# Optimization experiments

Measured on AMD Instinct MI355X. Metric: run time of the kernel, lower is better.

Reference implementation:

```python
import jax, jax.numpy as jnp
import numpy as np

N_NODES = 50000
N_EDGES = 800000
D = 128
BN_EPS = 1e-5


def setup_inputs() -> dict:
    key = jax.random.key(0)
    ks = jax.random.split(key, 8)
    scale = 1.0 / np.sqrt(D)
    return {
        "nfeat": jax.random.normal(ks[0], (N_NODES, D), dtype=jnp.float32),
        "efeat": jax.random.normal(ks[1], (N_EDGES, D), dtype=jnp.float32),
        "src": jax.random.randint(ks[2], (N_EDGES,), 0, N_NODES, dtype=jnp.int32),
        "dst": jax.random.randint(ks[3], (N_EDGES,), 0, N_NODES, dtype=jnp.int32),
        "W1": jax.random.normal(ks[4], (D, D), dtype=jnp.float32) * scale,
        "b1": jnp.zeros((D,), dtype=jnp.float32),
        "gamma": jnp.ones((D,), dtype=jnp.float32),
        "beta": jnp.zeros((D,), dtype=jnp.float32),
        "W2": jax.random.normal(ks[5], (D, D), dtype=jnp.float32) * scale,
        "b2": jnp.zeros((D,), dtype=jnp.float32),
        "We": jax.random.normal(ks[6], (D, D), dtype=jnp.float32) * scale,
        "be": jnp.zeros((D,), dtype=jnp.float32),
    }


def reference(nfeat, efeat, src, dst, W1, b1, gamma, beta, W2, b2, We, be):
    n = nfeat.shape[0]
    # GINConv, sum aggregator, eps=0: h = (1+eps)*x + sum_{j in N(i)} x_j
    agg = jax.ops.segment_sum(nfeat[src], dst, num_segments=n)  # [N, D]
    h = nfeat + agg
    # apply_func: Linear -> BatchNorm1d (training-mode batch stats) -> ReLU -> Linear
    h = h @ W1 + b1
    mu = jnp.mean(h, axis=0)
    var = jnp.mean(jnp.square(h - mu), axis=0)  # biased variance, as BatchNorm uses
    h = gamma * (h - mu) * jax.lax.rsqrt(var + BN_EPS) + beta
    h = jax.nn.relu(h)
    h = h @ W2 + b2
    # edge branch: linear on edge feats, scatter-sum to destination nodes, residual add
    e = efeat @ We + be                                          # [E, D]
    h_e = jax.ops.segment_sum(e, dst, num_segments=n)            # [N, D]
    return h + h_e
```

## Files before the change

### kernel.cpp

```cpp
#include <hip/hip_runtime.h>

#define D 128

typedef __attribute__((ext_vector_type(8))) short bf16x8;
typedef __attribute__((ext_vector_type(4))) float f32x4;

static __device__ __forceinline__ short f2bf(float f) {
    union { float f; unsigned u; } v; v.f = f;
    const unsigned r = v.u + 0x7FFFu + ((v.u >> 16) & 1u);
    return (short)(r >> 16);
}
static __device__ __forceinline__ float bf2f(short s) {
    union { unsigned u; float f; } v;
    v.u = ((unsigned)(unsigned short)s) << 16;
    return v.f;
}

__global__ __launch_bounds__(256) void k_prep(
    const float* __restrict__ nfeat, short* __restrict__ nfb,
    const float* __restrict__ W1, const float* __restrict__ W2,
    const float* __restrict__ We, short* __restrict__ Wt1,
    short* __restrict__ Wt2, short* __restrict__ Wte,
    int* __restrict__ cnt, float* __restrict__ stats,
    int N, int nbConv, int nbW)
{
    const int b = blockIdx.x, t = threadIdx.x;
    if (b < nbConv) {
        const int i = b * 256 + t;
        if (i < (N * D) / 4) {
            const float4 v = ((const float4*)nfeat)[i];
            short4 s;
            s.x = f2bf(v.x); s.y = f2bf(v.y); s.z = f2bf(v.z); s.w = f2bf(v.w);
            ((short4*)nfb)[i] = s;
        }
    } else if (b < nbConv + nbW) {
        const int i = (b - nbConv) * 256 + t;
        const int m = i >> 14;
        const int idx = i & 16383;
        const int k = idx >> 7, n = idx & 127;
        const float* W = (m == 0) ? W1 : (m == 1) ? W2 : We;
        short* Wt = (m == 0) ? Wt1 : (m == 1) ? Wt2 : Wte;
        Wt[n * 128 + k] = f2bf(W[k * 128 + n]);
    } else {
        const int i = (b - nbConv - nbW) * 256 + t;
        if (i * 4 < N) ((int4*)cnt)[i] = make_int4(0, 0, 0, 0);
        if (b == nbConv + nbW && t < 256) stats[t] = 0.f;
    }
}

__global__ void k_hist(const int* __restrict__ dst, int* __restrict__ cnt, int E) {
    const int base = (blockIdx.x * 256 + threadIdx.x) * 4;
    if (base + 3 < E) {
        const int4 d4 = *(const int4*)(dst + base);
        atomicAdd(&cnt[d4.x], 1);
        atomicAdd(&cnt[d4.y], 1);
        atomicAdd(&cnt[d4.z], 1);
        atomicAdd(&cnt[d4.w], 1);
    } else {
        for (int e = base; e < E; ++e) atomicAdd(&cnt[dst[e]], 1);
    }
}

__global__ __launch_bounds__(1024) void k_scan(
    const int* __restrict__ cnt, int* __restrict__ row_ptr,
    int* __restrict__ cursor, float* __restrict__ degf, int N)
{
    __shared__ int ws[17];
    const int t = threadIdx.x, lane = t & 63, wid = t >> 6;
    int carry = 0;
    const int ntiles = (N + 4095) / 4096;
    for (int tile = 0; tile < ntiles; ++tile) {
        const int base = tile * 4096 + t * 4;
        int4 v = make_int4(0, 0, 0, 0);
        if (base + 3 < N) v = *(const int4*)(cnt + base);
        else {
            if (base     < N) v.x = cnt[base];
            if (base + 1 < N) v.y = cnt[base + 1];
            if (base + 2 < N) v.z = cnt[base + 2];
            if (base + 3 < N) v.w = cnt[base + 3];
        }
        const int s = v.x + v.y + v.z + v.w;
        int incl = s;
        #pragma unroll
        for (int off = 1; off < 64; off <<= 1) {
            const int u = __shfl_up(incl, off);
            if (lane >= off) incl += u;
        }
        if (lane == 63) ws[wid] = incl;
        __syncthreads();
        if (t < 16) {
            const int wv = ws[t];
            int wincl = wv;
            #pragma unroll
            for (int off = 1; off < 16; off <<= 1) {
                const int u = __shfl_up(wincl, off);
                if (t >= off) wincl += u;
            }
            ws[t] = wincl - wv;
            if (t == 15) ws[16] = wincl;
        }
        __syncthreads();
        const int ex = carry + ws[wid] + (incl - s);
        if (base + 3 < N) {
            const int4 rp = make_int4(ex, ex + v.x, ex + v.x + v.y,
                                      ex + v.x + v.y + v.z);
            *(int4*)(row_ptr + base) = rp;
            *(int4*)(cursor + base)  = rp;
            *(float4*)(degf + base)  =
                make_float4((float)v.x, (float)v.y, (float)v.z, (float)v.w);
        } else {
            int run = ex;
            if (base < N)     { row_ptr[base]   = run; cursor[base]   = run; degf[base]   = (float)v.x; run += v.x; }
            if (base + 1 < N) { row_ptr[base+1] = run; cursor[base+1] = run; degf[base+1] = (float)v.y; run += v.y; }
            if (base + 2 < N) { row_ptr[base+2] = run; cursor[base+2] = run; degf[base+2] = (float)v.z; run += v.z; }
            if (base + 3 < N) { row_ptr[base+3] = run; cursor[base+3] = run; degf[base+3] = (float)v.w; }
        }
        carry += ws[16];
        __syncthreads();
    }
    if (t == 0) row_ptr[N] = carry;
}

__global__ void k_scatter(const int* __restrict__ src, const int* __restrict__ dst,
                          int* __restrict__ cursor,
                          int2* __restrict__ epair, int E) {
    const int base = (blockIdx.x * 256 + threadIdx.x) * 4;
    if (base + 3 < E) {
        const int4 d4 = *(const int4*)(dst + base);
        const int4 s4 = *(const int4*)(src + base);
        int p;
        p = atomicAdd(&cursor[d4.x], 1); epair[p] = make_int2(base + 0, s4.x);
        p = atomicAdd(&cursor[d4.y], 1); epair[p] = make_int2(base + 1, s4.y);
        p = atomicAdd(&cursor[d4.z], 1); epair[p] = make_int2(base + 2, s4.z);
        p = atomicAdd(&cursor[d4.w], 1); epair[p] = make_int2(base + 3, s4.w);
    } else {
        for (int e = base; e < E; ++e) {
            const int p = atomicAdd(&cursor[dst[e]], 1);
            epair[p] = make_int2(e, src[e]);
        }
    }
}

#define XS_STRIDE 136
__global__ __launch_bounds__(256) void k_gather_h1(
    const float* __restrict__ nfeat, const short* __restrict__ nfb,
    const float* __restrict__ efeat,
    const int* __restrict__ row_ptr, const int2* __restrict__ epair,
    const short* __restrict__ Wt1, const float* __restrict__ b1,
    short* __restrict__ agg_e, short* __restrict__ h1,
    float* __restrict__ stats, int N)
{
    __shared__ __attribute__((aligned(16))) short xs[64 * XS_STRIDE];
    const int t = threadIdx.x;
    const int lane = t & 63;
    const int w = t >> 6;
    const int h = lane >> 5;
    const int c = lane & 31;
    const int row0 = blockIdx.x * 64;

    for (int i = 0; i < 16; ++i) {
        const int nl = w * 16 + i;
        const int node = row0 + nl;
        if (node < N) {
            const int start = row_ptr[node];
            const int end   = row_ptr[node + 1];
            float4 an = make_float4(0.f, 0.f, 0.f, 0.f);
            float4 ae = make_float4(0.f, 0.f, 0.f, 0.f);
            for (int e = start + h; e < end; e += 2) {
                const int2 p = epair[e];
                const float4 ev = *(const float4*)(efeat + (size_t)p.x * D + c * 4);
                const short4 nv = *(const short4*)(nfb + (size_t)p.y * D + c * 4);
                ae.x += ev.x; ae.y += ev.y; ae.z += ev.z; ae.w += ev.w;
                an.x += bf2f(nv.x); an.y += bf2f(nv.y);
                an.z += bf2f(nv.z); an.w += bf2f(nv.w);
            }
            an.x += __shfl_xor(an.x, 32);
            an.y += __shfl_xor(an.y, 32);
            an.z += __shfl_xor(an.z, 32);
            an.w += __shfl_xor(an.w, 32);
            ae.x += __shfl_xor(ae.x, 32);
            ae.y += __shfl_xor(ae.y, 32);
            ae.z += __shfl_xor(ae.z, 32);
            ae.w += __shfl_xor(ae.w, 32);
            if (h == 0) {
                const float4 self = *(const float4*)(nfeat + (size_t)node * D + c * 4);
                short4 xv, ev2;
                xv.x = f2bf(self.x + an.x); xv.y = f2bf(self.y + an.y);
                xv.z = f2bf(self.z + an.z); xv.w = f2bf(self.w + an.w);
                ev2.x = f2bf(ae.x); ev2.y = f2bf(ae.y);
                ev2.z = f2bf(ae.z); ev2.w = f2bf(ae.w);
                *(short4*)(xs + nl * XS_STRIDE + c * 4) = xv;
                *(short4*)(agg_e + (size_t)node * D + c * 4) = ev2;
            }
        } else if (h == 0) {
            *(short4*)(xs + nl * XS_STRIDE + c * 4) = make_short4(0, 0, 0, 0);
        }
    }
    __syncthreads();

    const int l15 = lane & 15;
    const int kg  = lane >> 4;

    bf16x8 bfr[4][2];
    #pragma unroll
    for (int kt = 0; kt < 4; ++kt)
        #pragma unroll
        for (int cf = 0; cf < 2; ++cf)
            bfr[kt][cf] = *(const bf16x8*)(Wt1 + (w * 32 + cf * 16 + l15) * D +
                                           kt * 32 + kg * 8);

    f32x4 acc[4][2];
    #pragma unroll
    for (int rt = 0; rt < 4; ++rt) { acc[rt][0] = (f32x4)0.f; acc[rt][1] = (f32x4)0.f; }

    #pragma unroll
    for (int rt = 0; rt < 4; ++rt) {
        #pragma unroll
        for (int kt = 0; kt < 4; ++kt) {
            const bf16x8 a = *(const bf16x8*)(xs + (rt * 16 + l15) * XS_STRIDE +
                                              kt * 32 + kg * 8);
            acc[rt][0] = __builtin_amdgcn_mfma_f32_16x16x32_bf16(a, bfr[kt][0], acc[rt][0], 0, 0, 0);
            acc[rt][1] = __builtin_amdgcn_mfma_f32_16x16x32_bf16(a, bfr[kt][1], acc[rt][1], 0, 0, 0);
        }
    }

    const float bias0 = b1[w * 32 + l15];
    const float bias1 = b1[w * 32 + 16 + l15];
    float cs0 = 0.f, cq0 = 0.f, cs1 = 0.f, cq1 = 0.f;
    #pragma unroll
    for (int rt = 0; rt < 4; ++rt) {
        #pragma unroll
        for (int j = 0; j < 4; ++j) {
            const int row = row0 + rt * 16 + kg * 4 + j;
            if (row < N) {
                const float h0 = acc[rt][0][j] + bias0;
                const float hv = acc[rt][1][j] + bias1;
                h1[(size_t)row * D + w * 32 + l15]      = f2bf(h0);
                h1[(size_t)row * D + w * 32 + 16 + l15] = f2bf(hv);
                cs0 += h0; cq0 += h0 * h0;
                cs1 += hv; cq1 += hv * hv;
            }
        }
    }
    #pragma unroll
    for (int m = 16; m < 64; m <<= 1) {
        cs0 += __shfl_xor(cs0, m); cq0 += __shfl_xor(cq0, m);
        cs1 += __shfl_xor(cs1, m); cq1 += __shfl_xor(cq1, m);
    }
    if (lane < 16) {
        atomicAdd(stats + w * 32 + lane,            cs0);
        atomicAdd(stats + w * 32 + 16 + lane,       cs1);
        atomicAdd(stats + 128 + w * 32 + lane,      cq0);
        atomicAdd(stats + 128 + w * 32 + 16 + lane, cq1);
    }
}

__global__ __launch_bounds__(256) void k_out(const short* __restrict__ h1,
                                             const short* __restrict__ agg_e,
                                             const short* __restrict__ Wt2,
                                             const short* __restrict__ Wte,
                                             const float* __restrict__ stats,
                                             const float* __restrict__ gamma,
                                             const float* __restrict__ beta,
                                             const float* __restrict__ b2,
                                             const float* __restrict__ be,
                                             const float* __restrict__ degf,
                                             float* __restrict__ out, int N) {
    __shared__ float scs[128], shs[128];
    const int t = threadIdx.x;
    if (t < 128) {
        const float invN = 1.0f / (float)N;
        const float mu = stats[t] * invN;
        const float var = stats[128 + t] * invN - mu * mu;
        const float sc = gamma[t] * rsqrtf(var + 1e-5f);
        scs[t] = sc;
        shs[t] = beta[t] - mu * sc;
    }
    __syncthreads();

    const int lane = t & 63;
    const int w = t >> 6;
    const int l15 = lane & 15;
    const int kg = lane >> 4;
    const int row0 = blockIdx.x * 64;

    f32x4 acc[4][2];
    #pragma unroll
    for (int rt = 0; rt < 4; ++rt) { acc[rt][0] = (f32x4)0.f; acc[rt][1] = (f32x4)0.f; }

    bf16x8 bfr[4][2];

    #pragma unroll
    for (int kt = 0; kt < 4; ++kt)
        #pragma unroll
        for (int cf = 0; cf < 2; ++cf)
            bfr[kt][cf] = *(const bf16x8*)(Wt2 + (w * 32 + cf * 16 + l15) * D +
                                           kt * 32 + kg * 8);

    #pragma unroll
    for (int rt = 0; rt < 4; ++rt) {
        const int row = row0 + rt * 16 + l15;
        #pragma unroll
        for (int kt = 0; kt < 4; ++kt) {
            bf16x8 raw = (bf16x8)(short)0;
            if (row < N)
                raw = *(const bf16x8*)(h1 + (size_t)row * D + kt * 32 + kg * 8);
            const int k0 = kt * 32 + kg * 8;
            const float4 sa = *(const float4*)(scs + k0);
            const float4 sb = *(const float4*)(scs + k0 + 4);
            const float4 ha = *(const float4*)(shs + k0);
            const float4 hb = *(const float4*)(shs + k0 + 4);
            bf16x8 afr;
            afr[0] = f2bf(fmaxf(bf2f(raw[0]) * sa.x + ha.x, 0.f));
            afr[1] = f2bf(fmaxf(bf2f(raw[1]) * sa.y + ha.y, 0.f));
            afr[2] = f2bf(fmaxf(bf2f(raw[2]) * sa.z + ha.z, 0.f));
            afr[3] = f2bf(fmaxf(bf2f(raw[3]) * sa.w + ha.w, 0.f));
            afr[4] = f2bf(fmaxf(bf2f(raw[4]) * sb.x + hb.x, 0.f));
            afr[5] = f2bf(fmaxf(bf2f(raw[5]) * sb.y + hb.y, 0.f));
            afr[6] = f2bf(fmaxf(bf2f(raw[6]) * sb.z + hb.z, 0.f));
            afr[7] = f2bf(fmaxf(bf2f(raw[7]) * sb.w + hb.w, 0.f));
            acc[rt][0] = __builtin_amdgcn_mfma_f32_16x16x32_bf16(afr, bfr[kt][0], acc[rt][0], 0, 0, 0);
            acc[rt][1] = __builtin_amdgcn_mfma_f32_16x16x32_bf16(afr, bfr[kt][1], acc[rt][1], 0, 0, 0);
        }
    }

    #pragma unroll
    for (int kt = 0; kt < 4; ++kt)
        #pragma unroll
        for (int cf = 0; cf < 2; ++cf)
            bfr[kt][cf] = *(const bf16x8*)(Wte + (w * 32 + cf * 16 + l15) * D +
                                           kt * 32 + kg * 8);

    #pragma unroll
    for (int rt = 0; rt < 4; ++rt) {
        const int row = row0 + rt * 16 + l15;
        bf16x8 a0 = (bf16x8)(short)0, a1 = a0, a2 = a0, a3 = a0;
        if (row < N) {
            const short* ap = agg_e + (size_t)row * D + kg * 8;
            a0 = *(const bf16x8*)(ap);
            a1 = *(const bf16x8*)(ap + 32);
            a2 = *(const bf16x8*)(ap + 64);
            a3 = *(const bf16x8*)(ap + 96);
        }
        acc[rt][0] = __builtin_amdgcn_mfma_f32_16x16x32_bf16(a0, bfr[0][0], acc[rt][0], 0, 0, 0);
        acc[rt][1] = __builtin_amdgcn_mfma_f32_16x16x32_bf16(a0, bfr[0][1], acc[rt][1], 0, 0, 0);
        acc[rt][0] = __builtin_amdgcn_mfma_f32_16x16x32_bf16(a1, bfr[1][0], acc[rt][0], 0, 0, 0);
        acc[rt][1] = __builtin_amdgcn_mfma_f32_16x16x32_bf16(a1, bfr[1][1], acc[rt][1], 0, 0, 0);
        acc[rt][0] = __builtin_amdgcn_mfma_f32_16x16x32_bf16(a2, bfr[2][0], acc[rt][0], 0, 0, 0);
        acc[rt][1] = __builtin_amdgcn_mfma_f32_16x16x32_bf16(a2, bfr[2][1], acc[rt][1], 0, 0, 0);
        acc[rt][0] = __builtin_amdgcn_mfma_f32_16x16x32_bf16(a3, bfr[3][0], acc[rt][0], 0, 0, 0);
        acc[rt][1] = __builtin_amdgcn_mfma_f32_16x16x32_bf16(a3, bfr[3][1], acc[rt][1], 0, 0, 0);
    }

    const float b2_0 = b2[w * 32 + l15];
    const float b2_1 = b2[w * 32 + 16 + l15];
    const float be_0 = be[w * 32 + l15];
    const float be_1 = be[w * 32 + 16 + l15];
    #pragma unroll
    for (int rt = 0; rt < 4; ++rt) {
        const int rbase = row0 + rt * 16 + kg * 4;
        float dgv[4];
        if (rbase + 3 < N) {
            *(float4*)dgv = *(const float4*)(degf + rbase);
        } else {
            #pragma unroll
            for (int j = 0; j < 4; ++j)
                dgv[j] = (rbase + j < N) ? degf[rbase + j] : 0.f;
        }
        #pragma unroll
        for (int j = 0; j < 4; ++j) {
            const int row = rbase + j;
            if (row < N) {
                out[(size_t)row * D + w * 32 + l15] =
                    acc[rt][0][j] + b2_0 + dgv[j] * be_0;
                out[(size_t)row * D + w * 32 + 16 + l15] =
                    acc[rt][1][j] + b2_1 + dgv[j] * be_1;
            }
        }
    }
}

extern "C" void kernel_launch(void* const* d_in, const int* in_sizes, int n_in,
                              void* d_out, int out_size, void* d_ws, size_t ws_size,
                              hipStream_t stream) {
    const float* nfeat = (const float*)d_in[0];
    const float* efeat = (const float*)d_in[1];
    const int*   src   = (const int*)d_in[2];
    const int*   dst   = (const int*)d_in[3];
    const float* W1    = (const float*)d_in[4];
    const float* b1    = (const float*)d_in[5];
    const float* gamma = (const float*)d_in[6];
    const float* beta  = (const float*)d_in[7];
    const float* W2    = (const float*)d_in[8];
    const float* b2    = (const float*)d_in[9];
    const float* We    = (const float*)d_in[10];
    const float* be    = (const float*)d_in[11];
    float* out = (float*)d_out;

    const int N = in_sizes[0] / D;
    const int E = in_sizes[2];
    const size_t ND = (size_t)N * D;

    short* nfb    = (short*)d_ws;
    short* agg_e  = nfb + ND;
    short* h1     = agg_e + ND;
    short* Wt1    = h1 + ND;
    short* Wt2    = Wt1 + 16384;
    short* Wte    = Wt2 + 16384;
    float* stats  = (float*)(Wte + 16384);
    float* degf   = stats + 256;
    int*   row_ptr= (int*)(degf + N);
    int*   cursor = row_ptr + (N + 16);
    int*   cnt    = cursor + (N + 16);
    int2*  epair  = (int2*)(cnt + (N + 16));

    const int nbConv = ((N * D) / 4 + 255) / 256;
    const int nbW    = 192;
    const int nbZ    = (N / 4 + 255) / 256;
    const int ebl4   = (E / 4 + 255) / 256;
    const int nb     = (N + 63) / 64;

    k_prep<<<nbConv + nbW + nbZ, 256, 0, stream>>>(nfeat, nfb, W1, W2, We,
                                                   Wt1, Wt2, Wte, cnt, stats,
                                                   N, nbConv, nbW);
    k_hist<<<ebl4, 256, 0, stream>>>(dst, cnt, E);
    k_scan<<<1, 1024, 0, stream>>>(cnt, row_ptr, cursor, degf, N);
    k_scatter<<<ebl4, 256, 0, stream>>>(src, dst, cursor, epair, E);
    k_gather_h1<<<nb, 256, 0, stream>>>(nfeat, nfb, efeat, row_ptr, epair,
                                        Wt1, b1, agg_e, h1, stats, N);
    k_out<<<nb, 256, 0, stream>>>(h1, agg_e, Wt2, Wte, stats, gamma, beta,
                                  b2, be, degf, out, N);
}
```

Measured before the change: 343.7 us.

## Split fused gather+GEMM into separate one-node-per-wave gather and MFMA kernels

The fused gather-plus-Linear1 kernel is split in two. A gather kernel assigns one node per wave across many more blocks and unrolls the edge loop by two for more memory-level parallelism, writing the aggregated input to a global bf16 buffer. A separate MFMA kernel then reads that buffer to compute h1 in place, aliasing h1 to the same buffer. This trades an extra kernel launch and a global round-trip of the N×D bf16 tensor for better load balance and latency hiding in the memory-bound gather.

```diff
diff --git a/kernel.cpp b/kernel.cpp
--- a/kernel.cpp
+++ b/kernel.cpp
@@ -141,65 +141,79 @@
     }
 }
 
-#define XS_STRIDE 136
-__global__ __launch_bounds__(256) void k_gather_h1(
+__global__ __launch_bounds__(256) void k_gather(
     const float* __restrict__ nfeat, const short* __restrict__ nfb,
     const float* __restrict__ efeat,
     const int* __restrict__ row_ptr, const int2* __restrict__ epair,
-    const short* __restrict__ Wt1, const float* __restrict__ b1,
-    short* __restrict__ agg_e, short* __restrict__ h1,
-    float* __restrict__ stats, int N)
+    short* __restrict__ xbuf, short* __restrict__ agg_e, int N)
 {
-    __shared__ __attribute__((aligned(16))) short xs[64 * XS_STRIDE];
+    const int t = threadIdx.x;
+    const int lane = t & 63;
+    const int h = lane >> 5;
+    const int c = lane & 31;
+    const int node = blockIdx.x * 4 + (t >> 6);
+    if (node >= N) return;
+
+    const int start = row_ptr[node];
+    const int end   = row_ptr[node + 1];
+
+    float4 an = make_float4(0.f, 0.f, 0.f, 0.f);
+    float4 ae = make_float4(0.f, 0.f, 0.f, 0.f);
+    int e = start + h;
+    for (; e + 2 < end; e += 4) {
+        const int2 p0 = epair[e];
+        const int2 p1 = epair[e + 2];
+        const float4 ev0 = *(const float4*)(efeat + (size_t)p0.x * D + c * 4);
+        const short4 nv0 = *(const short4*)(nfb + (size_t)p0.y * D + c * 4);
+        const float4 ev1 = *(const float4*)(efeat + (size_t)p1.x * D + c * 4);
+        const short4 nv1 = *(const short4*)(nfb + (size_t)p1.y * D + c * 4);
+        ae.x += ev0.x + ev1.x; ae.y += ev0.y + ev1.y;
+        ae.z += ev0.z + ev1.z; ae.w += ev0.w + ev1.w;
+        an.x += bf2f(nv0.x) + bf2f(nv1.x);
+        an.y += bf2f(nv0.y) + bf2f(nv1.y);
+        an.z += bf2f(nv0.z) + bf2f(nv1.z);
+        an.w += bf2f(nv0.w) + bf2f(nv1.w);
+    }
+    if (e < end) {
+        const int2 p0 = epair[e];
+        const float4 ev0 = *(const float4*)(efeat + (size_t)p0.x * D + c * 4);
+        const short4 nv0 = *(const short4*)(nfb + (size_t)p0.y * D + c * 4);
+        ae.x += ev0.x; ae.y += ev0.y; ae.z += ev0.z; ae.w += ev0.w;
+        an.x += bf2f(nv0.x); an.y += bf2f(nv0.y);
+        an.z += bf2f(nv0.z); an.w += bf2f(nv0.w);
+    }
+    an.x += __shfl_xor(an.x, 32);
+    an.y += __shfl_xor(an.y, 32);
+    an.z += __shfl_xor(an.z, 32);
+    an.w += __shfl_xor(an.w, 32);
+    ae.x += __shfl_xor(ae.x, 32);
+    ae.y += __shfl_xor(ae.y, 32);
+    ae.z += __shfl_xor(ae.z, 32);
+    ae.w += __shfl_xor(ae.w, 32);
+
+    if (h == 0) {
+        const float4 self = *(const float4*)(nfeat + (size_t)node * D + c * 4);
+        short4 xv, ev2;
+        xv.x = f2bf(self.x + an.x); xv.y = f2bf(self.y + an.y);
+        xv.z = f2bf(self.z + an.z); xv.w = f2bf(self.w + an.w);
+        ev2.x = f2bf(ae.x); ev2.y = f2bf(ae.y);
+        ev2.z = f2bf(ae.z); ev2.w = f2bf(ae.w);
+        *(short4*)(xbuf  + (size_t)node * D + c * 4) = xv;
+        *(short4*)(agg_e + (size_t)node * D + c * 4) = ev2;
+    }
+}
+
+__global__ __launch_bounds__(256) void k_h1(const short* xbuf,
+                                            const short* __restrict__ Wt1,
+                                            const float* __restrict__ b1,
+                                            short* h1,
+                                            float* __restrict__ stats, int N) {
     const int t = threadIdx.x;
     const int lane = t & 63;
     const int w = t >> 6;
-    const int h = lane >> 5;
-    const int c = lane & 31;
+    const int l15 = lane & 15;
+    const int kg = lane >> 4;
     const int row0 = blockIdx.x * 64;
-
-    for (int i = 0; i < 16; ++i) {
-        const int nl = w * 16 + i;
-        const int node = row0 + nl;
-        if (node < N) {
-            const int start = row_ptr[node];
-            const int end   = row_ptr[node + 1];
-            float4 an = make_float4(0.f, 0.f, 0.f, 0.f);
-            float4 ae = make_float4(0.f, 0.f, 0.f, 0.f);
-            for (int e = start + h; e < end; e += 2) {
-                const int2 p = epair[e];
-                const float4 ev = *(const float4*)(efeat + (size_t)p.x * D + c * 4);
-                const short4 nv = *(const short4*)(nfb + (size_t)p.y * D + c * 4);
-                ae.x += ev.x; ae.y += ev.y; ae.z += ev.z; ae.w += ev.w;
-                an.x += bf2f(nv.x); an.y += bf2f(nv.y);
-                an.z += bf2f(nv.z); an.w += bf2f(nv.w);
-            }
-            an.x += __shfl_xor(an.x, 32);
-            an.y += __shfl_xor(an.y, 32);
-            an.z += __shfl_xor(an.z, 32);
-            an.w += __shfl_xor(an.w, 32);
-            ae.x += __shfl_xor(ae.x, 32);
-            ae.y += __shfl_xor(ae.y, 32);
-            ae.z += __shfl_xor(ae.z, 32);
-            ae.w += __shfl_xor(ae.w, 32);
-            if (h == 0) {
-                const float4 self = *(const float4*)(nfeat + (size_t)node * D + c * 4);
-                short4 xv, ev2;
-                xv.x = f2bf(self.x + an.x); xv.y = f2bf(self.y + an.y);
-                xv.z = f2bf(self.z + an.z); xv.w = f2bf(self.w + an.w);
-                ev2.x = f2bf(ae.x); ev2.y = f2bf(ae.y);
-                ev2.z = f2bf(ae.z); ev2.w = f2bf(ae.w);
-                *(short4*)(xs + nl * XS_STRIDE + c * 4) = xv;
-                *(short4*)(agg_e + (size_t)node * D + c * 4) = ev2;
-            }
-        } else if (h == 0) {
-            *(short4*)(xs + nl * XS_STRIDE + c * 4) = make_short4(0, 0, 0, 0);
-        }
-    }
-    __syncthreads();
-
-    const int l15 = lane & 15;
-    const int kg  = lane >> 4;
 
     bf16x8 bfr[4][2];
     #pragma unroll
@@ -215,13 +229,23 @@
 
     #pragma unroll
     for (int rt = 0; rt < 4; ++rt) {
-        #pragma unroll
-        for (int kt = 0; kt < 4; ++kt) {
-            const bf16x8 a = *(const bf16x8*)(xs + (rt * 16 + l15) * XS_STRIDE +
-                                              kt * 32 + kg * 8);
-            acc[rt][0] = __builtin_amdgcn_mfma_f32_16x16x32_bf16(a, bfr[kt][0], acc[rt][0], 0, 0, 0);
-            acc[rt][1] = __builtin_amdgcn_mfma_f32_16x16x32_bf16(a, bfr[kt][1], acc[rt][1], 0, 0, 0);
-        }
+        const int row = row0 + rt * 16 + l15;
+        bf16x8 a0 = (bf16x8)(short)0, a1 = a0, a2 = a0, a3 = a0;
+        if (row < N) {
+            const short* xp = xbuf + (size_t)row * D + kg * 8;
+            a0 = *(const bf16x8*)(xp);
+            a1 = *(const bf16x8*)(xp + 32);
+            a2 = *(const bf16x8*)(xp + 64);
+            a3 = *(const bf16x8*)(xp + 96);
+        }
+        acc[rt][0] = __builtin_amdgcn_mfma_f32_16x16x32_bf16(a0, bfr[0][0], acc[rt][0], 0, 0, 0);
+        acc[rt][1] = __builtin_amdgcn_mfma_f32_16x16x32_bf16(a0, bfr[0][1], acc[rt][1], 0, 0, 0);
+        acc[rt][0] = __builtin_amdgcn_mfma_f32_16x16x32_bf16(a1, bfr[1][0], acc[rt][0], 0, 0, 0);
+        acc[rt][1] = __builtin_amdgcn_mfma_f32_16x16x32_bf16(a1, bfr[1][1], acc[rt][1], 0, 0, 0);
+        acc[rt][0] = __builtin_amdgcn_mfma_f32_16x16x32_bf16(a2, bfr[2][0], acc[rt][0], 0, 0, 0);
+        acc[rt][1] = __builtin_amdgcn_mfma_f32_16x16x32_bf16(a2, bfr[2][1], acc[rt][1], 0, 0, 0);
+        acc[rt][0] = __builtin_amdgcn_mfma_f32_16x16x32_bf16(a3, bfr[3][0], acc[rt][0], 0, 0, 0);
+        acc[rt][1] = __builtin_amdgcn_mfma_f32_16x16x32_bf16(a3, bfr[3][1], acc[rt][1], 0, 0, 0);
     }
 
     const float bias0 = b1[w * 32 + l15];
@@ -402,9 +426,10 @@
     const size_t ND = (size_t)N * D;
 
     short* nfb    = (short*)d_ws;
-    short* agg_e  = nfb + ND;
-    short* h1     = agg_e + ND;
-    short* Wt1    = h1 + ND;
+    short* xbuf   = nfb + ND;
+    short* h1     = xbuf;
+    short* agg_e  = xbuf + ND;
+    short* Wt1    = agg_e + ND;
     short* Wt2    = Wt1 + 16384;
     short* Wte    = Wt2 + 16384;
     float* stats  = (float*)(Wte + 16384);
@@ -426,8 +451,9 @@
     k_hist<<<ebl4, 256, 0, stream>>>(dst, cnt, E);
     k_scan<<<1, 1024, 0, stream>>>(cnt, row_ptr, cursor, degf, N);
     k_scatter<<<ebl4, 256, 0, stream>>>(src, dst, cursor, epair, E);
-    k_gather_h1<<<nb, 256, 0, stream>>>(nfeat, nfb, efeat, row_ptr, epair,
-                                        Wt1, b1, agg_e, h1, stats, N);
+    k_gather<<<(N + 3) / 4, 256, 0, stream>>>(nfeat, nfb, efeat, row_ptr, epair,
+                                              xbuf, agg_e, N);
+    k_h1<<<nb, 256, 0, stream>>>(xbuf, Wt1, b1, h1, stats, N);
     k_out<<<nb, 256, 0, stream>>>(h1, agg_e, Wt2, Wte, stats, gamma, beta,
                                   b2, be, degf, out, N);
 }
```

Measured after the change: 285.8 us. -16.9%, faster.
